# Kernel tuning notes

Hardware: AMD Instinct MI355X
Metric: run time of the kernel (lower is better)

Reference implementation:

```python
import jax, jax.numpy as jnp
import numpy as np

WINDOW = 512  # window_size from init_kwargs


def _sliding_window_attn(q, k, v, window):
    # q,k,v: [B, S, H, D]; each query attends to keys j with i-window < j <= i (causal band)
    B, S, H, D = q.shape
    W = window
    NB = S // W  # S chosen divisible by W
    qb = q.reshape(B, NB, W, H, D)
    kb = k.reshape(B, NB, W, H, D)
    vb = v.reshape(B, NB, W, H, D)
    # previous block of keys/values (zeros for block 0, masked out below)
    kprev = jnp.pad(kb, ((0, 0), (1, 0), (0, 0), (0, 0), (0, 0)))[:, :NB]
    vprev = jnp.pad(vb, ((0, 0), (1, 0), (0, 0), (0, 0), (0, 0)))[:, :NB]
    kcat = jnp.concatenate([kprev, kb], axis=2)  # [B, NB, 2W, H, D]
    vcat = jnp.concatenate([vprev, vb], axis=2)
    qi = jnp.arange(W)
    kj = jnp.arange(2 * W) - W  # key position relative to block start
    rel = kj[None, :] - qi[:, None]  # [W, 2W]
    win_mask = (rel <= 0) & (rel > -W)  # causal window of size W (incl. self)
    blk = jnp.arange(NB)
    valid_key = (blk[:, None, None] > 0) | (kj[None, None, :] >= 0)  # block 0 has no prev
    mask = win_mask[None] & valid_key  # [NB, W, 2W]
    scale = 1.0 / np.sqrt(D).astype(np.float32)
    scores = jnp.einsum('bnqhd,bnkhd->bhnqk', qb, kcat) * scale  # [B,H,NB,W,2W]
    scores = jnp.where(mask[None, None], scores, jnp.finfo(scores.dtype).min)
    probs = jax.nn.softmax(scores, axis=-1)
    out = jnp.einsum('bhnqk,bnkhd->bnqhd', probs, vcat)  # [B,NB,W,H,D]
    return out.reshape(B, S, H, D)


def setup_inputs() -> dict:
    B, S, H, D = 2, 8192, 8, 64
    root = jax.random.key(0)
    k1, k2, k3, k4, k5 = jax.random.split(root, 5)
    query = jax.random.normal(k1, (B, S, H, D), dtype=jnp.float32)
    key = jax.random.normal(k2, (B, S, H, D), dtype=jnp.float32)
    value = jax.random.normal(k3, (B, S, H, D), dtype=jnp.float32)
    W_out = jax.random.normal(k4, (H * D, H * D), dtype=jnp.float32) * (1.0 / np.sqrt(H * D))
    b_out = jax.random.normal(k5, (H * D,), dtype=jnp.float32) * 0.01
    return {'query': query, 'key': key, 'value': value, 'W_out': W_out, 'b_out': b_out}


def reference(query, key, value, W_out, b_out):
    B, S, H, D = query.shape
    # seq_len (8192) > window_size (512) -> sliding-window branch of the module
    attn = _sliding_window_attn(query, key, value, WINDOW)
    flat = attn.reshape(B, S, H * D)
    # out_proj (nn.Linear); dropout=0.0 is identity; no attention_mask
    return flat @ W_out.T + b_out
```

## Files before the change

kernel.cpp:

```cpp
#include <hip/hip_runtime.h>

#define B_ 2
#define S_ 8192
#define H_ 8
#define D_ 64
#define HD_ 512
#define WIN_ 512

typedef __bf16 bf16x8 __attribute__((ext_vector_type(8)));
typedef float f32x4 __attribute__((ext_vector_type(4)));
typedef unsigned short u16;
typedef unsigned int u32;

__device__ __forceinline__ u16 f2bf(float f) {
  u32 u = __float_as_uint(f);
  u += 0x7FFFu + ((u >> 16) & 1u);
  return (u16)(u >> 16);
}

__device__ __forceinline__ bf16x8 cvt8s(const float* p, float s) {
  const float4 a = *(const float4*)p;
  const float4 b = *(const float4*)(p + 4);
  union { u16 s[8]; bf16x8 v; } r;
  r.s[0] = f2bf(a.x * s); r.s[1] = f2bf(a.y * s); r.s[2] = f2bf(a.z * s); r.s[3] = f2bf(a.w * s);
  r.s[4] = f2bf(b.x * s); r.s[5] = f2bf(b.y * s); r.s[6] = f2bf(b.z * s); r.s[7] = f2bf(b.w * s);
  return r.v;
}

#define MFMA(a, b, c) __builtin_amdgcn_mfma_f32_16x16x32_bf16(a, b, c, 0, 0, 0)

__global__ __launch_bounds__(256) void vtrans_kernel(const float* __restrict__ v,
                                                     u16* __restrict__ vt) {
  const int t = threadIdx.x;
  const int s0 = (blockIdx.x & (S_ / 64 - 1)) * 64;
  const int bh = blockIdx.x >> 7;
  const int b = bh >> 3, h = bh & 7;
  __shared__ float tile[64][65];
#pragma unroll
  for (int it = 0; it < 16; ++it) {
    int idx = it * 256 + t;
    int r = idx >> 6, c = idx & 63;
    tile[r][c] = v[((size_t)(b * S_ + s0 + r) * H_ + h) * D_ + c];
  }
  __syncthreads();
#pragma unroll
  for (int it = 0; it < 16; ++it) {
    int idx = it * 256 + t;
    int dd = idx >> 6, c = idx & 63;
    vt[((size_t)(b * H_ + h) * D_ + dd) * S_ + s0 + c] = f2bf(tile[c][dd]);
  }
}

__global__ __launch_bounds__(256) void cvt_kernel(const float* __restrict__ in,
                                                  u16* __restrict__ out, int n4) {
  int i = blockIdx.x * 256 + threadIdx.x;
  if (i < n4) {
    float4 f = ((const float4*)in)[i];
    ushort4 r;
    r.x = f2bf(f.x); r.y = f2bf(f.y); r.z = f2bf(f.z); r.w = f2bf(f.w);
    ((ushort4*)out)[i] = r;
  }
}

__global__ __launch_bounds__(512) void attn_kernel(const float* __restrict__ q,
                                                   const u16* __restrict__ kb,
                                                   const u16* __restrict__ vt,
                                                   u16* __restrict__ attn) {
  const int tid = threadIdx.x;
  const int lane = tid & 63;
  const int wave = tid >> 6;
  const int lg = lane >> 4;
  const int lj = lane & 15;
  const int bid = (int)blockIdx.x;
  const int swz = (bid & 7) * 128 + (bid >> 3);
  const int qc = swz & 63;
  const int bh = swz >> 6;
  const int b = bh >> 3, h = bh & 7;
  const int q0blk = qc * 128;
  const int q0w = q0blk + wave * 16;

  __shared__ __align__(16) u16 klds0[32 * 64], klds1[32 * 64];
  __shared__ __align__(16) u16 vlds0[64 * 32], vlds1[64 * 32];
  __shared__ __align__(16) u16 plds[8][16][32];

  const float qscale = 0.125f * 1.4426950408889634f;
  bf16x8 aq0, aq1;
  {
    const float* qrow = q + ((size_t)(b * S_ + q0w + lj) * H_ + h) * D_;
    aq0 = cvt8s(qrow + lg * 8, qscale);
    aq1 = cvt8s(qrow + 32 + lg * 8, qscale);
  }

  f32x4 o0 = {0.f, 0.f, 0.f, 0.f}, o1 = o0, o2 = o0, o3 = o0;
  float lacc[4] = {0.f, 0.f, 0.f, 0.f};

  const int tbw = (q0w >= WIN_) ? ((q0w - (WIN_ - 1)) >> 5) : 0;
  const int tew = (q0w + 15) >> 5;
  const int tbu = (q0blk >= WIN_) ? ((q0blk - (WIN_ - 1)) >> 5) : 0;
  const int teu = (q0blk + 127) >> 5;
  const bool wmask = (q0w >= WIN_);

  const bool isK = (wave < 4);
  const u16* gbase;
  size_t gstep;
  u16 *l0, *l1;
  if (isK) {
    const int chunk = wave * 64 + lane;
    const int r = chunk >> 3, c = chunk & 7;
    gbase = kb + ((size_t)(b * S_ + r) * H_ + h) * D_ + c * 8;
    gstep = (size_t)32 * HD_;
    const int dst = r * 64 + ((c * 8) ^ ((r & 7) << 3));
    l0 = klds0 + dst; l1 = klds1 + dst;
  } else {
    const int chunk = (wave - 4) * 64 + lane;
    const int d = chunk >> 2, c = chunk & 3;
    gbase = vt + ((size_t)(b * H_ + h) * D_ + d) * S_ + c * 8;
    gstep = 32;
    const int dst = d * 32 + ((c * 8) ^ ((d & 3) << 3));
    l0 = vlds0 + dst; l1 = vlds1 + dst;
  }

  const int ko0 = lj * 64 + ((lg * 8) ^ ((lj & 7) << 3));
  const int ko1 = lj * 64 + (((32 + lg * 8)) ^ ((lj & 7) << 3));
  const int vo = lj * 32 + ((lg * 8) ^ ((lj & 3) << 3));

  {
    uint4 g0 = *(const uint4*)(gbase + gstep * tbu);
    *(uint4*)l0 = g0;
  }
  uint4 greg;
  if (tbu < teu) greg = *(const uint4*)(gbase + gstep * (tbu + 1));
  __syncthreads();

  int cur = 0;
  for (int t = tbu; t <= teu; ++t) {
    if (t >= tbw && t <= tew) {
      const u16* K = cur ? klds1 : klds0;
      const u16* V = cur ? vlds1 : vlds0;
      bf16x8 k00 = *(const bf16x8*)(K + ko0);
      bf16x8 k01 = *(const bf16x8*)(K + ko1);
      bf16x8 k10 = *(const bf16x8*)(K + ko0 + 1024);
      bf16x8 k11 = *(const bf16x8*)(K + ko1 + 1024);

      f32x4 sA = {0.f, 0.f, 0.f, 0.f}, sB = sA;
      sA = MFMA(aq0, k00, sA);
      sA = MFMA(aq1, k01, sA);
      sB = MFMA(aq0, k10, sB);
      sB = MFMA(aq1, k11, sB);

      const bool edge = (t == tew) || (wmask && t == tbw);
      float pa[4], pb[4];
#pragma unroll
      for (int r = 0; r < 4; ++r) {
        float ea = __builtin_amdgcn_exp2f(sA[r]);
        float eb = __builtin_amdgcn_exp2f(sB[r]);
        if (edge) {
          const int qpos = q0w + lg * 4 + r;
          const int kA = 32 * t + lj, kB = kA + 16;
          const bool okA = (kA <= qpos) && (kA > qpos - WIN_);
          const bool okB = (kB <= qpos) && (kB > qpos - WIN_);
          ea = okA ? ea : 0.f;
          eb = okB ? eb : 0.f;
        }
        pa[r] = ea; pb[r] = eb;
        lacc[r] += ea + eb;
      }

      u16* ps = &plds[wave][0][0];
#pragma unroll
      for (int r = 0; r < 4; ++r) {
        ps[(lg * 4 + r) * 32 + lj] = f2bf(pa[r]);
        ps[(lg * 4 + r) * 32 + 16 + lj] = f2bf(pb[r]);
      }
      bf16x8 ap = *(const bf16x8*)(ps + lj * 32 + lg * 8);

      bf16x8 v0 = *(const bf16x8*)(V + vo);
      bf16x8 v1 = *(const bf16x8*)(V + vo + 512);
      bf16x8 v2 = *(const bf16x8*)(V + vo + 1024);
      bf16x8 v3 = *(const bf16x8*)(V + vo + 1536);
      o0 = MFMA(ap, v0, o0);
      o1 = MFMA(ap, v1, o1);
      o2 = MFMA(ap, v2, o2);
      o3 = MFMA(ap, v3, o3);
    }

    if (t < teu) {
      u16* dst = cur ? l0 : l1;
      *(uint4*)dst = greg;
    }
    __syncthreads();
    if (t + 1 < teu) greg = *(const uint4*)(gbase + gstep * (t + 2));
    cur ^= 1;
  }

#pragma unroll
  for (int r = 0; r < 4; ++r) {
    float l = lacc[r];
    l += __shfl_xor(l, 1);
    l += __shfl_xor(l, 2);
    l += __shfl_xor(l, 4);
    l += __shfl_xor(l, 8);
    const float inv = 1.0f / l;
    const int row = q0w + lg * 4 + r;
    u16* orow = attn + (size_t)(b * S_ + row) * HD_ + h * D_;
    orow[lj] = f2bf(o0[r] * inv);
    orow[16 + lj] = f2bf(o1[r] * inv);
    orow[32 + lj] = f2bf(o2[r] * inv);
    orow[48 + lj] = f2bf(o3[r] * inv);
  }
}

__global__ __launch_bounds__(512) void gemm_kernel(const u16* __restrict__ A,
                                                   const u16* __restrict__ Wb,
                                                   const float* __restrict__ bias,
                                                   float* __restrict__ out) {
  const int tid = threadIdx.x;
  const int lane = tid & 63;
  const int wave = tid >> 6;
  const int lg = lane >> 4, lj = lane & 15;
  const int phys = (int)blockIdx.x;
  const int swz = (phys & 7) * 32 + (phys >> 3);
  const int rb = swz >> 1, cb = swz & 1;
  const int wr = wave >> 2, wc = wave & 3;
  const int row0 = rb * 128;
  const int col0 = cb * 256 + wc * 64;

  __shared__ __align__(16) u16 alds[2][128 * 64];

  const int srow = tid >> 3;
  const int skc = tid & 7;
  const u16* ag0 = A + (size_t)(row0 + srow) * HD_ + skc * 8;
  const u16* ag1 = A + (size_t)(row0 + 64 + srow) * HD_ + skc * 8;
  const int dst0 = srow * 64 + ((skc * 8) ^ ((srow & 7) << 3));
  const int dst1 = (64 + srow) * 64 + ((skc * 8) ^ ((srow & 7) << 3));

  f32x4 acc[4][4];
#pragma unroll
  for (int fr = 0; fr < 4; ++fr)
#pragma unroll
    for (int fc = 0; fc < 4; ++fc) acc[fr][fc] = (f32x4){0.f, 0.f, 0.f, 0.f};

  *(uint4*)(&alds[0][dst0]) = *(const uint4*)ag0;
  *(uint4*)(&alds[0][dst1]) = *(const uint4*)ag1;
  __syncthreads();

  uint4 pre0, pre1;
  int cur = 0;
  for (int kt = 0; kt < HD_; kt += 64) {
    if (kt + 64 < HD_) {
      pre0 = *(const uint4*)(ag0 + kt + 64);
      pre1 = *(const uint4*)(ag1 + kt + 64);
    }
    const u16* Abuf = alds[cur];
#pragma unroll
    for (int ks = 0; ks < 2; ++ks) {
      bf16x8 fa[4], fb[4];
#pragma unroll
      for (int fr = 0; fr < 4; ++fr) {
        const int rr = wr * 64 + fr * 16 + lj;
        fa[fr] = *(const bf16x8*)(Abuf + rr * 64 + ((ks * 32 + lg * 8) ^ ((lj & 7) << 3)));
      }
#pragma unroll
      for (int fc = 0; fc < 4; ++fc)
        fb[fc] = *(const bf16x8*)(Wb + (size_t)(col0 + fc * 16 + lj) * HD_ + kt + ks * 32 + lg * 8);
#pragma unroll
      for (int fr = 0; fr < 4; ++fr)
#pragma unroll
        for (int fc = 0; fc < 4; ++fc)
          acc[fr][fc] = MFMA(fa[fr], fb[fc], acc[fr][fc]);
    }
    if (kt + 64 < HD_) {
      u16* db = alds[cur ^ 1];
      *(uint4*)(&db[dst0]) = pre0;
      *(uint4*)(&db[dst1]) = pre1;
    }
    __syncthreads();
    cur ^= 1;
  }

#pragma unroll
  for (int fc = 0; fc < 4; ++fc) {
    const float bv = bias[col0 + fc * 16 + lj];
#pragma unroll
    for (int fr = 0; fr < 4; ++fr) {
#pragma unroll
      for (int r = 0; r < 4; ++r) {
        const int row = row0 + wr * 64 + fr * 16 + lg * 4 + r;
        out[(size_t)row * HD_ + col0 + fc * 16 + lj] = acc[fr][fc][r] + bv;
      }
    }
  }
}

extern "C" void kernel_launch(void* const* d_in, const int* in_sizes, int n_in,
                              void* d_out, int out_size, void* d_ws, size_t ws_size,
                              hipStream_t stream) {
  const float* q = (const float*)d_in[0];
  const float* k = (const float*)d_in[1];
  const float* v = (const float*)d_in[2];
  const float* w = (const float*)d_in[3];
  const float* bias = (const float*)d_in[4];
  float* out = (float*)d_out;

  char* ws = (char*)d_ws;
  u16* vt = (u16*)ws;
  u16* kbb = (u16*)(ws + 16777216);
  u16* attn = (u16*)(ws + 33554432);
  u16* wb = (u16*)(ws + 50331648);

  hipLaunchKernelGGL(vtrans_kernel, dim3(2048), dim3(256), 0, stream, v, vt);
  hipLaunchKernelGGL(cvt_kernel, dim3(8192), dim3(256), 0, stream, k, kbb, 2097152);
  hipLaunchKernelGGL(cvt_kernel, dim3(256), dim3(256), 0, stream, w, wb, 65536);
  hipLaunchKernelGGL(attn_kernel, dim3(1024), dim3(512), 0, stream, q, kbb, vt, attn);
  hipLaunchKernelGGL(gemm_kernel, dim3(256), dim3(512), 0, stream, attn, wb, bias, out);
}
```

Measured before the change: 94.74 us.

## Give each attention wave two query sub-tiles to reuse K/V LDS loads

The attention block drops from 8 to 4 waves, and each wave now handles 32 query rows as two 16-row sub-tiles. The K and V fragments read from LDS each step are shared by both sub-tiles, which halves LDS read traffic per query. The XOR swizzle is replaced by padded LDS rows, and the probability conversion to bf16 changes from round-to-nearest to truncation. In exchange, each wave holds more registers and does more serial work, and with fewer waves per block there is less latency hiding.

```diff
diff --git a/kernel.cpp b/kernel.cpp
--- a/kernel.cpp
+++ b/kernel.cpp
@@ -62,7 +62,7 @@
   }
 }
 
-__global__ __launch_bounds__(512) void attn_kernel(const float* __restrict__ q,
+__global__ __launch_bounds__(256) void attn_kernel(const float* __restrict__ q,
                                                    const u16* __restrict__ kb,
                                                    const u16* __restrict__ vt,
                                                    u16* __restrict__ attn) {
@@ -77,136 +77,161 @@
   const int bh = swz >> 6;
   const int b = bh >> 3, h = bh & 7;
   const int q0blk = qc * 128;
-  const int q0w = q0blk + wave * 16;
-
-  __shared__ __align__(16) u16 klds0[32 * 64], klds1[32 * 64];
-  __shared__ __align__(16) u16 vlds0[64 * 32], vlds1[64 * 32];
-  __shared__ __align__(16) u16 plds[8][16][32];
+  const int q0w = q0blk + wave * 32;
+
+  __shared__ __align__(16) u16 klds[2][32 * 72];
+  __shared__ __align__(16) u16 vlds[2][64 * 40];
+  __shared__ __align__(16) u16 plds[4][2][16 * 40];
 
   const float qscale = 0.125f * 1.4426950408889634f;
-  bf16x8 aq0, aq1;
-  {
-    const float* qrow = q + ((size_t)(b * S_ + q0w + lj) * H_ + h) * D_;
-    aq0 = cvt8s(qrow + lg * 8, qscale);
-    aq1 = cvt8s(qrow + 32 + lg * 8, qscale);
-  }
-
-  f32x4 o0 = {0.f, 0.f, 0.f, 0.f}, o1 = o0, o2 = o0, o3 = o0;
-  float lacc[4] = {0.f, 0.f, 0.f, 0.f};
-
-  const int tbw = (q0w >= WIN_) ? ((q0w - (WIN_ - 1)) >> 5) : 0;
-  const int tew = (q0w + 15) >> 5;
+  bf16x8 aq[2][2];
+#pragma unroll
+  for (int qs = 0; qs < 2; ++qs) {
+    const float* qrow = q + ((size_t)(b * S_ + q0w + qs * 16 + lj) * H_ + h) * D_;
+    aq[qs][0] = cvt8s(qrow + lg * 8, qscale);
+    aq[qs][1] = cvt8s(qrow + 32 + lg * 8, qscale);
+  }
+
+  f32x4 o[2][4];
+#pragma unroll
+  for (int qs = 0; qs < 2; ++qs)
+#pragma unroll
+    for (int g = 0; g < 4; ++g) o[qs][g] = (f32x4){0.f, 0.f, 0.f, 0.f};
+  float lacc[2][4] = {};
+
+  int tbq[2], teq[2];
+  bool wm[2];
+#pragma unroll
+  for (int qs = 0; qs < 2; ++qs) {
+    const int qq = q0w + qs * 16;
+    wm[qs] = (qq >= WIN_);
+    tbq[qs] = wm[qs] ? ((qq - (WIN_ - 1)) >> 5) : 0;
+    teq[qs] = (qq + 15) >> 5;
+  }
   const int tbu = (q0blk >= WIN_) ? ((q0blk - (WIN_ - 1)) >> 5) : 0;
   const int teu = (q0blk + 127) >> 5;
-  const bool wmask = (q0w >= WIN_);
-
-  const bool isK = (wave < 4);
-  const u16* gbase;
+
+  const u16 *g0, *g1;
   size_t gstep;
-  u16 *l0, *l1;
-  if (isK) {
-    const int chunk = wave * 64 + lane;
-    const int r = chunk >> 3, c = chunk & 7;
-    gbase = kb + ((size_t)(b * S_ + r) * H_ + h) * D_ + c * 8;
+  int dst0, dst1;
+  bool stK = (tid < 128);
+  if (stK) {
+    const int ch0 = tid, ch1 = tid + 128;
+    const int r0 = ch0 >> 3, c0 = ch0 & 7;
+    const int r1 = ch1 >> 3, c1 = ch1 & 7;
+    g0 = kb + ((size_t)(b * S_ + r0) * H_ + h) * D_ + c0 * 8;
+    g1 = kb + ((size_t)(b * S_ + r1) * H_ + h) * D_ + c1 * 8;
     gstep = (size_t)32 * HD_;
-    const int dst = r * 64 + ((c * 8) ^ ((r & 7) << 3));
-    l0 = klds0 + dst; l1 = klds1 + dst;
+    dst0 = r0 * 72 + c0 * 8;
+    dst1 = r1 * 72 + c1 * 8;
   } else {
-    const int chunk = (wave - 4) * 64 + lane;
-    const int d = chunk >> 2, c = chunk & 3;
-    gbase = vt + ((size_t)(b * H_ + h) * D_ + d) * S_ + c * 8;
+    const int u = tid - 128;
+    const int ch0 = u, ch1 = u + 128;
+    const int d0 = ch0 >> 2, c0 = ch0 & 3;
+    const int d1 = ch1 >> 2, c1 = ch1 & 3;
+    g0 = vt + ((size_t)(b * H_ + h) * D_ + d0) * S_ + c0 * 8;
+    g1 = vt + ((size_t)(b * H_ + h) * D_ + d1) * S_ + c1 * 8;
     gstep = 32;
-    const int dst = d * 32 + ((c * 8) ^ ((d & 3) << 3));
-    l0 = vlds0 + dst; l1 = vlds1 + dst;
-  }
-
-  const int ko0 = lj * 64 + ((lg * 8) ^ ((lj & 7) << 3));
-  const int ko1 = lj * 64 + (((32 + lg * 8)) ^ ((lj & 7) << 3));
-  const int vo = lj * 32 + ((lg * 8) ^ ((lj & 3) << 3));
+    dst0 = d0 * 40 + c0 * 8;
+    dst1 = d1 * 40 + c1 * 8;
+  }
+
+  const int ko0 = lj * 72 + lg * 8;
+  const int ko1 = lj * 72 + 32 + lg * 8;
+  const int kof = 16 * 72;
+  const int po = lj * 40 + lg * 8;
 
   {
-    uint4 g0 = *(const uint4*)(gbase + gstep * tbu);
-    *(uint4*)l0 = g0;
-  }
-  uint4 greg;
-  if (tbu < teu) greg = *(const uint4*)(gbase + gstep * (tbu + 1));
+    u16* kl = stK ? klds[0] : vlds[0];
+    *(uint4*)(kl + dst0) = *(const uint4*)(g0 + gstep * tbu);
+    *(uint4*)(kl + dst1) = *(const uint4*)(g1 + gstep * tbu);
+  }
+  uint4 greg0, greg1;
+  if (tbu < teu) {
+    greg0 = *(const uint4*)(g0 + gstep * (tbu + 1));
+    greg1 = *(const uint4*)(g1 + gstep * (tbu + 1));
+  }
   __syncthreads();
 
   int cur = 0;
   for (int t = tbu; t <= teu; ++t) {
-    if (t >= tbw && t <= tew) {
-      const u16* K = cur ? klds1 : klds0;
-      const u16* V = cur ? vlds1 : vlds0;
+    if (t >= tbq[0] && t <= teq[1]) {
+      const u16* K = klds[cur];
+      const u16* V = vlds[cur];
       bf16x8 k00 = *(const bf16x8*)(K + ko0);
       bf16x8 k01 = *(const bf16x8*)(K + ko1);
-      bf16x8 k10 = *(const bf16x8*)(K + ko0 + 1024);
-      bf16x8 k11 = *(const bf16x8*)(K + ko1 + 1024);
-
-      f32x4 sA = {0.f, 0.f, 0.f, 0.f}, sB = sA;
-      sA = MFMA(aq0, k00, sA);
-      sA = MFMA(aq1, k01, sA);
-      sB = MFMA(aq0, k10, sB);
-      sB = MFMA(aq1, k11, sB);
-
-      const bool edge = (t == tew) || (wmask && t == tbw);
-      float pa[4], pb[4];
-#pragma unroll
-      for (int r = 0; r < 4; ++r) {
-        float ea = __builtin_amdgcn_exp2f(sA[r]);
-        float eb = __builtin_amdgcn_exp2f(sB[r]);
-        if (edge) {
-          const int qpos = q0w + lg * 4 + r;
-          const int kA = 32 * t + lj, kB = kA + 16;
-          const bool okA = (kA <= qpos) && (kA > qpos - WIN_);
-          const bool okB = (kB <= qpos) && (kB > qpos - WIN_);
-          ea = okA ? ea : 0.f;
-          eb = okB ? eb : 0.f;
+      bf16x8 k10 = *(const bf16x8*)(K + ko0 + kof);
+      bf16x8 k11 = *(const bf16x8*)(K + ko1 + kof);
+      bf16x8 v0 = *(const bf16x8*)(V + (lj) * 40 + lg * 8);
+      bf16x8 v1 = *(const bf16x8*)(V + (16 + lj) * 40 + lg * 8);
+      bf16x8 v2 = *(const bf16x8*)(V + (32 + lj) * 40 + lg * 8);
+      bf16x8 v3 = *(const bf16x8*)(V + (48 + lj) * 40 + lg * 8);
+
+#pragma unroll
+      for (int qs = 0; qs < 2; ++qs) {
+        if (t < tbq[qs] || t > teq[qs]) continue;
+        f32x4 sA = {0.f, 0.f, 0.f, 0.f}, sB = sA;
+        sA = MFMA(aq[qs][0], k00, sA);
+        sA = MFMA(aq[qs][1], k01, sA);
+        sB = MFMA(aq[qs][0], k10, sB);
+        sB = MFMA(aq[qs][1], k11, sB);
+
+        const bool edge = (t == teq[qs]) || (wm[qs] && t == tbq[qs]);
+        u16* ps = &plds[wave][qs][0];
+#pragma unroll
+        for (int r = 0; r < 4; ++r) {
+          float ea = __builtin_amdgcn_exp2f(sA[r]);
+          float eb = __builtin_amdgcn_exp2f(sB[r]);
+          if (edge) {
+            const int qpos = q0w + qs * 16 + lg * 4 + r;
+            const int kA = 32 * t + lj, kB = kA + 16;
+            const bool okA = (kA <= qpos) && (kA > qpos - WIN_);
+            const bool okB = (kB <= qpos) && (kB > qpos - WIN_);
+            ea = okA ? ea : 0.f;
+            eb = okB ? eb : 0.f;
+          }
+          lacc[qs][r] += ea + eb;
+          ps[(lg * 4 + r) * 40 + lj] = (u16)(__float_as_uint(ea) >> 16);
+          ps[(lg * 4 + r) * 40 + 16 + lj] = (u16)(__float_as_uint(eb) >> 16);
         }
-        pa[r] = ea; pb[r] = eb;
-        lacc[r] += ea + eb;
+        bf16x8 ap = *(const bf16x8*)(ps + po);
+        o[qs][0] = MFMA(ap, v0, o[qs][0]);
+        o[qs][1] = MFMA(ap, v1, o[qs][1]);
+        o[qs][2] = MFMA(ap, v2, o[qs][2]);
+        o[qs][3] = MFMA(ap, v3, o[qs][3]);
       }
-
-      u16* ps = &plds[wave][0][0];
-#pragma unroll
-      for (int r = 0; r < 4; ++r) {
-        ps[(lg * 4 + r) * 32 + lj] = f2bf(pa[r]);
-        ps[(lg * 4 + r) * 32 + 16 + lj] = f2bf(pb[r]);
-      }
-      bf16x8 ap = *(const bf16x8*)(ps + lj * 32 + lg * 8);
-
-      bf16x8 v0 = *(const bf16x8*)(V + vo);
-      bf16x8 v1 = *(const bf16x8*)(V + vo + 512);
-      bf16x8 v2 = *(const bf16x8*)(V + vo + 1024);
-      bf16x8 v3 = *(const bf16x8*)(V + vo + 1536);
-      o0 = MFMA(ap, v0, o0);
-      o1 = MFMA(ap, v1, o1);
-      o2 = MFMA(ap, v2, o2);
-      o3 = MFMA(ap, v3, o3);
     }
 
     if (t < teu) {
-      u16* dst = cur ? l0 : l1;
-      *(uint4*)dst = greg;
+      u16* dl = stK ? klds[cur ^ 1] : vlds[cur ^ 1];
+      *(uint4*)(dl + dst0) = greg0;
+      *(uint4*)(dl + dst1) = greg1;
     }
     __syncthreads();
-    if (t + 1 < teu) greg = *(const uint4*)(gbase + gstep * (t + 2));
+    if (t + 1 < teu) {
+      greg0 = *(const uint4*)(g0 + gstep * (t + 2));
+      greg1 = *(const uint4*)(g1 + gstep * (t + 2));
+    }
     cur ^= 1;
   }
 
 #pragma unroll
-  for (int r = 0; r < 4; ++r) {
-    float l = lacc[r];
-    l += __shfl_xor(l, 1);
-    l += __shfl_xor(l, 2);
-    l += __shfl_xor(l, 4);
-    l += __shfl_xor(l, 8);
-    const float inv = 1.0f / l;
-    const int row = q0w + lg * 4 + r;
-    u16* orow = attn + (size_t)(b * S_ + row) * HD_ + h * D_;
-    orow[lj] = f2bf(o0[r] * inv);
-    orow[16 + lj] = f2bf(o1[r] * inv);
-    orow[32 + lj] = f2bf(o2[r] * inv);
-    orow[48 + lj] = f2bf(o3[r] * inv);
+  for (int qs = 0; qs < 2; ++qs) {
+#pragma unroll
+    for (int r = 0; r < 4; ++r) {
+      float l = lacc[qs][r];
+      l += __shfl_xor(l, 1);
+      l += __shfl_xor(l, 2);
+      l += __shfl_xor(l, 4);
+      l += __shfl_xor(l, 8);
+      const float inv = 1.0f / l;
+      const int row = q0w + qs * 16 + lg * 4 + r;
+      u16* orow = attn + (size_t)(b * S_ + row) * HD_ + h * D_;
+      orow[lj] = f2bf(o[qs][0][r] * inv);
+      orow[16 + lj] = f2bf(o[qs][1][r] * inv);
+      orow[32 + lj] = f2bf(o[qs][2][r] * inv);
+      orow[48 + lj] = f2bf(o[qs][3][r] * inv);
+    }
   }
 }
 
@@ -311,6 +336,6 @@
   hipLaunchKernelGGL(vtrans_kernel, dim3(2048), dim3(256), 0, stream, v, vt);
   hipLaunchKernelGGL(cvt_kernel, dim3(8192), dim3(256), 0, stream, k, kbb, 2097152);
   hipLaunchKernelGGL(cvt_kernel, dim3(256), dim3(256), 0, stream, w, wb, 65536);
-  hipLaunchKernelGGL(attn_kernel, dim3(1024), dim3(512), 0, stream, q, kbb, vt, attn);
+  hipLaunchKernelGGL(attn_kernel, dim3(1024), dim3(256), 0, stream, q, kbb, vt, attn);
   hipLaunchKernelGGL(gemm_kernel, dim3(256), dim3(512), 0, stream, attn, wb, bias, out);
 }
```

Result: slower. 103.9 us (+9.6%).
